# Kernel tuning notes

Measured on AMD Instinct MI355X. Metric: run time of the kernel, lower is better.

Reference implementation:

```python
import jax, jax.numpy as jnp
import numpy as np

D_MODEL = 1024
NUM_HEADS = 16
D_FF = 4096
EPS = 1e-5


def setup_inputs() -> dict:
    key = jax.random.key(0)
    ks = jax.random.split(key, 8)
    B, S, D = 4, 2048, D_MODEL
    s = 1.0 / np.sqrt(D)
    return {
        "x": jax.random.normal(ks[0], (B, S, D), jnp.float32),
        "ln1_w": jnp.ones((D,), jnp.float32),
        "ln2_w": jnp.ones((D,), jnp.float32),
        "wq": jax.random.normal(ks[1], (D, D), jnp.float32) * s,
        "wk": jax.random.normal(ks[2], (D, D), jnp.float32) * s,
        "wv": jax.random.normal(ks[3], (D, D), jnp.float32) * s,
        "wo": jax.random.normal(ks[4], (D, D), jnp.float32) * s,
        "w1": jax.random.normal(ks[5], (D_FF, D), jnp.float32) * s,
        "w2": jax.random.normal(ks[6], (D, D_FF), jnp.float32) * (1.0 / np.sqrt(D_FF)),
    }


def rmsnorm(a, w):
    # (a * w) / sqrt(mean(a^2) + eps)  -- matches torch module exactly
    denom = jnp.sqrt(jnp.mean(jnp.square(a), axis=-1, keepdims=True) + EPS)
    return a * w / denom


def attention(x, wq, wk, wv, wo):
    B, S, D = x.shape
    H, dk = NUM_HEADS, D // NUM_HEADS
    q = (x @ wq.T).reshape(B, S, H, dk).transpose(0, 2, 1, 3)  # B H S dk
    k = (x @ wk.T).reshape(B, S, H, dk).transpose(0, 2, 1, 3)
    v = (x @ wv.T).reshape(B, S, H, dk).transpose(0, 2, 1, 3)
    scores = jnp.einsum("bhqd,bhkd->bhqk", q, k) / np.sqrt(dk)
    causal = jnp.triu(jnp.ones((S, S), bool), k=1)
    scores = jnp.where(causal, -jnp.inf, scores)
    probs = jax.nn.softmax(scores, axis=-1)
    out = jnp.einsum("bhqk,bhkd->bhqd", probs, v)
    out = out.transpose(0, 2, 1, 3).reshape(B, S, D)
    return out @ wo.T


def ffn(x, w1, w2):
    h = x @ w1.T
    h = 0.5 * h * (1.0 + jax.lax.erf(h / np.sqrt(2.0).astype(np.float32)))
    return h @ w2.T


def reference(x, ln1_w, ln2_w, wq, wk, wv, wo, w1, w2):
    y = x + attention(rmsnorm(x, ln1_w), wq, wk, wv, wo)
    return y + ffn(rmsnorm(y, ln2_w), w1, w2)
```

## Files before the change

kernel.cpp:

```cpp
#include <hip/hip_runtime.h>

#define DM    1024
#define DFF   4096
#define SEQ   2048
#define BATCH 4
#define NROWS (BATCH * SEQ)
#define HEADS 16
#define DKH   64
#define KSTR  (2 * DM)

typedef __attribute__((ext_vector_type(4))) float          f32x4;
typedef __attribute__((ext_vector_type(8))) __bf16         bf16x8;
typedef __attribute__((ext_vector_type(8))) unsigned short u16x8;
typedef __attribute__((ext_vector_type(4))) unsigned short u16x4;

static __device__ __forceinline__ unsigned short f2bf(float f) {
  unsigned u = __builtin_bit_cast(unsigned, f);
  u += 0x7fffu + ((u >> 16) & 1u);
  return (unsigned short)(u >> 16);
}

__global__ void k_f2bf(const float* __restrict__ in, unsigned short* __restrict__ out, int n4) {
  int i = blockIdx.x * blockDim.x + threadIdx.x;
  if (i >= n4) return;
  float4 v = reinterpret_cast<const float4*>(in)[i];
  ushort4 o;
  o.x = f2bf(v.x); o.y = f2bf(v.y); o.z = f2bf(v.z); o.w = f2bf(v.w);
  reinterpret_cast<ushort4*>(out)[i] = o;
}

__global__ __launch_bounds__(256) void k_rmsnorm(const float* __restrict__ x,
                                                 const float* __restrict__ w,
                                                 unsigned short* __restrict__ out) {
  const int row = blockIdx.x;
  const float4 v = reinterpret_cast<const float4*>(x + (size_t)row * DM)[threadIdx.x];
  float ss = v.x * v.x + v.y * v.y + v.z * v.z + v.w * v.w;
#pragma unroll
  for (int off = 32; off > 0; off >>= 1) ss += __shfl_down(ss, off);
  __shared__ float red[4];
  if ((threadIdx.x & 63) == 0) red[threadIdx.x >> 6] = ss;
  __syncthreads();
  const float tot  = red[0] + red[1] + red[2] + red[3];
  const float rden = rsqrtf(tot * (1.0f / DM) + 1e-5f);
  const float4 wv = reinterpret_cast<const float4*>(w)[threadIdx.x];
  ushort4 o;
  o.x = f2bf(v.x * wv.x * rden);
  o.y = f2bf(v.y * wv.y * rden);
  o.z = f2bf(v.z * wv.z * rden);
  o.w = f2bf(v.w * wv.w * rden);
  reinterpret_cast<ushort4*>(out + (size_t)row * DM)[threadIdx.x] = o;
}

template <int EPI, int TN, int BK>
__global__ __launch_bounds__(256, 2) void k_gemm_nt(const unsigned short* __restrict__ A,
                                                    const unsigned short* __restrict__ B,
                                                    void* __restrict__ Cv,
                                                    const float* __restrict__ res,
                                                    int M, int N, int K) {
  constexpr int NW = TN / 128;
  alignas(16) __shared__ unsigned short As[2][128 * BK];
  alignas(16) __shared__ unsigned short Bs[2][128 * NW * BK];
  const int t  = threadIdx.x;
  const int w  = t >> 6;
  const int l  = t & 63;
  const int wr = w >> 1, wc = w & 1;
  const int lr = l & 15, lk = l >> 4;

  const unsigned bid = blockIdx.y * gridDim.x + blockIdx.x;
  const unsigned cpx = (gridDim.x * gridDim.y) >> 3;
  const unsigned sw  = (bid & 7) * cpx + (bid >> 3);
  const int m0 = (int)(sw / gridDim.x) * 128;
  const int n0 = (int)(sw % gridDim.x) * TN;

  auto stage = [&](int buf, int k0) {
    if constexpr (BK == 32) {
      const int srow = t >> 2;
      const int sgr  = (t & 3) ^ (srow & 3);
#pragma unroll
      for (int r = 0; r < 2; ++r) {
        const unsigned short* ga = A + (size_t)(m0 + r * 64 + srow) * K + k0 + 8 * sgr;
        __builtin_amdgcn_global_load_lds((__attribute__((address_space(1))) void*)ga,
                                         (__attribute__((address_space(3))) void*)(&As[buf][r * 2048 + w * 512]),
                                         16, 0, 0);
      }
#pragma unroll
      for (int r = 0; r < 2 * NW; ++r) {
        const unsigned short* gb = B + (size_t)(n0 + r * 64 + srow) * K + k0 + 8 * sgr;
        __builtin_amdgcn_global_load_lds((__attribute__((address_space(1))) void*)gb,
                                         (__attribute__((address_space(3))) void*)(&Bs[buf][r * 2048 + w * 512]),
                                         16, 0, 0);
      }
    } else {
      const int srow8 = l >> 3;
      const int g     = l & 7;
#pragma unroll
      for (int i = 0; i < 4; ++i) {
        const int row = i * 32 + w * 8 + srow8;
        const int sg  = g ^ (row & 7);
        const unsigned short* ga = A + (size_t)(m0 + row) * K + k0 + 8 * sg;
        __builtin_amdgcn_global_load_lds((__attribute__((address_space(1))) void*)ga,
                                         (__attribute__((address_space(3))) void*)(&As[buf][i * 2048 + w * 512]),
                                         16, 0, 0);
        const unsigned short* gb = B + (size_t)(n0 + row) * K + k0 + 8 * sg;
        __builtin_amdgcn_global_load_lds((__attribute__((address_space(1))) void*)gb,
                                         (__attribute__((address_space(3))) void*)(&Bs[buf][i * 2048 + w * 512]),
                                         16, 0, 0);
      }
    }
  };

  f32x4 acc[4][4 * NW] = {};

  stage(0, 0);
  const int nIt = K / BK;
  for (int it = 0; it < nIt; ++it) {
    const int buf = it & 1;
    __syncthreads();
    if (it + 1 < nIt) stage(buf ^ 1, (it + 1) * BK);

    if constexpr (BK == 32) {
      bf16x8 af[4], bf[4 * NW];
#pragma unroll
      for (int m = 0; m < 4; ++m)
        af[m] = *reinterpret_cast<const bf16x8*>(
            &As[buf][(wr * 64 + m * 16 + lr) * 32 + 8 * (lk ^ (lr & 3))]);
#pragma unroll
      for (int n = 0; n < 4 * NW; ++n)
        bf[n] = *reinterpret_cast<const bf16x8*>(
            &Bs[buf][(wc * 64 * NW + n * 16 + lr) * 32 + 8 * (lk ^ (lr & 3))]);
#pragma unroll
      for (int m = 0; m < 4; ++m)
#pragma unroll
        for (int n = 0; n < 4 * NW; ++n)
          acc[m][n] = __builtin_amdgcn_mfma_f32_16x16x32_bf16(af[m], bf[n], acc[m][n], 0, 0, 0);
    } else {
#pragma unroll
      for (int kk = 0; kk < 2; ++kk) {
        bf16x8 af[4], bf[4];
#pragma unroll
        for (int m = 0; m < 4; ++m)
          af[m] = *reinterpret_cast<const bf16x8*>(
              &As[buf][(wr * 64 + m * 16 + lr) * 64 + 8 * ((4 * kk + lk) ^ (lr & 7))]);
#pragma unroll
        for (int n = 0; n < 4; ++n)
          bf[n] = *reinterpret_cast<const bf16x8*>(
              &Bs[buf][(wc * 64 + n * 16 + lr) * 64 + 8 * ((4 * kk + lk) ^ (lr & 7))]);
#pragma unroll
        for (int m = 0; m < 4; ++m)
#pragma unroll
          for (int n = 0; n < 4; ++n)
            acc[m][n] = __builtin_amdgcn_mfma_f32_16x16x32_bf16(af[m], bf[n], acc[m][n], 0, 0, 0);
      }
    }
  }

#pragma unroll
  for (int m = 0; m < 4; ++m) {
#pragma unroll
    for (int n = 0; n < 4 * NW; ++n) {
#pragma unroll
      for (int r = 0; r < 4; ++r) {
        const size_t row = (size_t)(m0 + wr * 64 + m * 16 + lk * 4 + r);
        const size_t col = (size_t)(n0 + wc * 64 * NW + n * 16 + lr);
        const float a = acc[m][n][r];
        if constexpr (EPI == 0) {
          ((unsigned short*)Cv)[row * N + col] = f2bf(a);
        } else if constexpr (EPI == 1) {
          ((float*)Cv)[row * N + col] = a + res[row * N + col];
        } else if constexpr (EPI == 2) {
          const float h2 = a * a;
          const float e  = exp2f(a * (2.30221535f + 0.10295355f * h2));
          const float g  = a - a / (e + 1.0f);
          ((unsigned short*)Cv)[row * N + col] = f2bf(g);
        } else {
          const float sc = (col < DM) ? 0.18033688011f : 1.0f;
          ((unsigned short*)Cv)[row * N + col] = f2bf(a * sc);
        }
      }
    }
  }
}

__global__ __launch_bounds__(256, 3) void k_attn(const unsigned short* __restrict__ QK,
                                                 const unsigned short* __restrict__ VT,
                                                 unsigned short* __restrict__ O) {
  const int h   = blockIdx.x;
  const int qtA = blockIdx.y;
  const int qtB = 31 - qtA;
  const int b   = blockIdx.z;
  const int t  = threadIdx.x, w = t >> 6, l = t & 63;
  const int lr = l & 15, lk = l >> 4;
  const size_t rowB = (size_t)b * SEQ;
  const int hoff  = h * DKH;
  const int qw2[2] = { qtA * 64 + 16 * w, qtB * 64 + 16 * w };

  alignas(16) __shared__ unsigned short Ks[2][64 * 64];
  alignas(16) __shared__ unsigned short Vt[2][64 * 64];
  alignas(16) __shared__ unsigned short Ps[2][4][16 * 64];

  char* const KsB = (char*)Ks;
  char* const VtB = (char*)Vt;

  auto stage = [&](int buf, int kb2) {
#pragma unroll
    for (int half = 0; half < 2; ++half) {
      const int srow = w * 16 + half * 8 + (l >> 3);
      const int sgr  = (l & 7) ^ (srow & 7);
      const unsigned short* gk = QK + (size_t)(rowB + kb2 + srow) * KSTR + DM + hoff + 8 * sgr;
      __builtin_amdgcn_global_load_lds((__attribute__((address_space(1))) void*)gk,
                                       (__attribute__((address_space(3))) void*)(KsB + buf * 8192 + w * 2048 + half * 1024),
                                       16, 0, 0);
      const unsigned short* gv = VT + (size_t)(hoff + srow) * NROWS + rowB + kb2 + 8 * sgr;
      __builtin_amdgcn_global_load_lds((__attribute__((address_space(1))) void*)gv,
                                       (__attribute__((address_space(3))) void*)(VtB + buf * 8192 + w * 2048 + half * 1024),
                                       16, 0, 0);
    }
  };

  bf16x8 qf[2][2];
#pragma unroll
  for (int s = 0; s < 2; ++s)
#pragma unroll
    for (int kk = 0; kk < 2; ++kk)
      qf[s][kk] = *reinterpret_cast<const bf16x8*>(
          QK + (rowB + qw2[s] + lr) * KSTR + hoff + 32 * kk + 8 * lk);

  f32x4 oacc[2][4] = {};
  float mrun[2] = {-1e30f, -1e30f};
  float lrun[2] = {0.0f, 0.0f};

  const int ktmax = qtB;
  stage(0, 0);
  for (int kt = 0; kt <= ktmax; ++kt) {
    const int kbase = kt * 64;
    const int cur   = kt & 1;
    __syncthreads();
    if (kt < ktmax) stage(cur ^ 1, kbase + 64);
    const char* Kc = KsB + cur * 8192;
    const char* Vc = VtB + cur * 8192;

    const bool act[2] = { kbase <= qw2[0] + 15, kbase <= qw2[1] + 15 };

    f32x4 sacc[2][4] = {};
#pragma unroll
    for (int tt = 0; tt < 4; ++tt) {
      bf16x8 kf0 = *reinterpret_cast<const bf16x8*>(Kc + (16 * tt + lr) * 128 + 16 * ((lk + 0) ^ (lr & 7)));
      bf16x8 kf1 = *reinterpret_cast<const bf16x8*>(Kc + (16 * tt + lr) * 128 + 16 * ((lk + 4) ^ (lr & 7)));
#pragma unroll
      for (int s = 0; s < 2; ++s) {
        if (!act[s]) continue;
        sacc[s][tt] = __builtin_amdgcn_mfma_f32_16x16x32_bf16(kf0, qf[s][0], sacc[s][tt], 0, 0, 0);
        sacc[s][tt] = __builtin_amdgcn_mfma_f32_16x16x32_bf16(kf1, qf[s][1], sacc[s][tt], 0, 0, 0);
      }
    }

#pragma unroll
    for (int s = 0; s < 2; ++s) {
      if (!act[s]) continue;
      const int qw = qw2[s];
      char* const PsSB = (char*)(Ps[s][w]);
      const int qg = qw + lr;
      float sv[4][4];
      if (kbase + 63 > qw) {
#pragma unroll
        for (int tt = 0; tt < 4; ++tt)
#pragma unroll
          for (int r = 0; r < 4; ++r) {
            const int kg = kbase + 16 * tt + 4 * lk + r;
            sv[tt][r] = (kg > qg) ? -1e30f : sacc[s][tt][r];
          }
      } else {
#pragma unroll
        for (int tt = 0; tt < 4; ++tt)
#pragma unroll
          for (int r = 0; r < 4; ++r) sv[tt][r] = sacc[s][tt][r];
      }
      float tm = sv[0][0];
#pragma unroll
      for (int tt = 0; tt < 4; ++tt)
#pragma unroll
        for (int r = 0; r < 4; ++r) tm = fmaxf(tm, sv[tt][r]);
      tm = fmaxf(tm, __shfl_xor(tm, 16));
      tm = fmaxf(tm, __shfl_xor(tm, 32));
      float mref = mrun[s];
      if (__any(tm > mref + 8.0f)) {
        const float mnew  = fmaxf(mref, tm);
        const float alpha = exp2f(mref - mnew);
#pragma unroll
        for (int r = 0; r < 4; ++r) {
          const float ar = __shfl(alpha, 4 * lk + r);
#pragma unroll
          for (int dn = 0; dn < 4; ++dn) oacc[s][dn][r] *= ar;
        }
        lrun[s] *= alpha;
        mrun[s] = mnew;
        mref = mnew;
      }
      float ts = 0.0f;
      unsigned short pb[4][4];
#pragma unroll
      for (int tt = 0; tt < 4; ++tt)
#pragma unroll
        for (int r = 0; r < 4; ++r) {
          const float p = exp2f(sv[tt][r] - mref);
          ts += p;
          pb[tt][r] = __builtin_bit_cast(unsigned short, static_cast<__bf16>(p));
        }
      ts += __shfl_xor(ts, 16);
      ts += __shfl_xor(ts, 32);
      lrun[s] += ts;
#pragma unroll
      for (int tt = 0; tt < 4; ++tt) {
        u16x4 pw = {pb[tt][0], pb[tt][1], pb[tt][2], pb[tt][3]};
        *reinterpret_cast<u16x4*>(
            PsSB + lr * 128 + ((32 * tt + 8 * lk) ^ (16 * (lr & 7)))) = pw;
      }
    }

    asm volatile("" ::: "memory");

#pragma unroll
    for (int kk = 0; kk < 2; ++kk) {
      bf16x8 vf[4];
#pragma unroll
      for (int dn = 0; dn < 4; ++dn)
        vf[dn] = *reinterpret_cast<const bf16x8*>(
            Vc + (16 * dn + lr) * 128 + 16 * ((4 * kk + lk) ^ (lr & 7)));
#pragma unroll
      for (int s = 0; s < 2; ++s) {
        if (!act[s]) continue;
        char* const PsSB = (char*)(Ps[s][w]);
        bf16x8 pa = *reinterpret_cast<const bf16x8*>(
            PsSB + lr * 128 + ((64 * kk + 16 * lk) ^ (16 * (lr & 7))));
#pragma unroll
        for (int dn = 0; dn < 4; ++dn)
          oacc[s][dn] = __builtin_amdgcn_mfma_f32_16x16x32_bf16(pa, vf[dn], oacc[s][dn], 0, 0, 0);
      }
    }

    asm volatile("" ::: "memory");
  }

#pragma unroll
  for (int s = 0; s < 2; ++s)
#pragma unroll
    for (int r = 0; r < 4; ++r) {
      const float li = 1.0f / __shfl(lrun[s], 4 * lk + r);
      const size_t row = rowB + qw2[s] + 4 * lk + r;
#pragma unroll
      for (int dn = 0; dn < 4; ++dn)
        O[row * DM + hoff + 16 * dn + lr] = f2bf(oacc[s][dn][r] * li);
    }
}

extern "C" void kernel_launch(void* const* d_in, const int* in_sizes, int n_in,
                              void* d_out, int out_size, void* d_ws, size_t ws_size,
                              hipStream_t stream) {
  const float* x   = (const float*)d_in[0];
  const float* ln1 = (const float*)d_in[1];
  const float* ln2 = (const float*)d_in[2];
  const float* wq  = (const float*)d_in[3];
  const float* wk  = (const float*)d_in[4];
  const float* wv  = (const float*)d_in[5];
  const float* wo  = (const float*)d_in[6];
  const float* w1  = (const float*)d_in[7];
  const float* w2  = (const float*)d_in[8];

  char* ws = (char*)d_ws;
  size_t off = 0;
  auto take = [&](size_t bytes) { void* p = ws + off; off += bytes; return p; };
  unsigned short* wqkb = (unsigned short*)take((size_t)2 * DM * DM * 2);
  unsigned short* wvb  = (unsigned short*)take((size_t)DM * DM * 2);
  unsigned short* wob  = (unsigned short*)take((size_t)DM * DM * 2);
  unsigned short* w1b  = (unsigned short*)take((size_t)DFF * DM * 2);
  unsigned short* w2b  = (unsigned short*)take((size_t)DM * DFF * 2);
  unsigned short* qk   = (unsigned short*)take((size_t)NROWS * 2 * DM * 2);
  unsigned short* xn   = (unsigned short*)take((size_t)NROWS * DM * 2);
  unsigned short* vtb  = (unsigned short*)take((size_t)DM * NROWS * 2);
  float*          yb   = (float*)take((size_t)NROWS * DM * 4);
  unsigned short* hb   = (unsigned short*)take((size_t)NROWS * DFF * 2);
  unsigned short* yn   = qk;

  auto cvt = [&](const float* src, unsigned short* dst, size_t n) {
    int n4 = (int)(n / 4);
    k_f2bf<<<dim3((n4 + 255) / 256), dim3(256), 0, stream>>>(src, dst, n4);
  };
  cvt(wq, wqkb, (size_t)DM * DM);
  cvt(wk, wqkb + (size_t)DM * DM, (size_t)DM * DM);
  cvt(wv, wvb, (size_t)DM * DM);
  cvt(wo, wob, (size_t)DM * DM);
  cvt(w1, w1b, (size_t)DFF * DM);
  cvt(w2, w2b, (size_t)DM * DFF);

  k_rmsnorm<<<dim3(NROWS), dim3(256), 0, stream>>>(x, ln1, xn);

  k_gemm_nt<3, 256, 32><<<dim3(2 * DM / 256, NROWS / 128), dim3(256), 0, stream>>>(
      xn, wqkb, qk, nullptr, NROWS, 2 * DM, DM);

  k_gemm_nt<0, 128, 64><<<dim3(NROWS / 128, DM / 128), dim3(256), 0, stream>>>(
      wvb, xn, vtb, nullptr, DM, NROWS, DM);

  k_attn<<<dim3(HEADS, 16, BATCH), dim3(256), 0, stream>>>(qk, vtb, xn);

  k_gemm_nt<1, 128, 64><<<dim3(DM / 128, NROWS / 128), dim3(256), 0, stream>>>(
      xn, wob, yb, x, NROWS, DM, DM);

  k_rmsnorm<<<dim3(NROWS), dim3(256), 0, stream>>>(yb, ln2, yn);

  k_gemm_nt<2, 256, 32><<<dim3(DFF / 256, NROWS / 128), dim3(256), 0, stream>>>(
      yn, w1b, hb, nullptr, NROWS, DFF, DM);
  k_gemm_nt<1, 128, 64><<<dim3(DM / 128, NROWS / 128), dim3(256), 0, stream>>>(
      hb, w2b, (float*)d_out, yb, NROWS, DM, DFF);
}
```

Before: 391.0 us.

## Batch weight conversions into one launch, raise MFMA priority, tree-reduce softmax

Merges the six per-weight fp32-to-bf16 conversion launches into a single kernel that finds each thread's job from a cumulative-size table, removing per-launch overhead and tail effects. In the attention kernel, wraps the QK and PV MFMA sections in s_setprio raises so the scheduler favours matrix work across waves. It also rewrites the row-max and row-sum reductions as balanced trees to shorten dependency chains. The tree sum reorders float additions, which can change rounding slightly.

New measurement: 378.8 us. 1.03x faster.

```diff
diff --git a/kernel.cpp b/kernel.cpp
--- a/kernel.cpp
+++ b/kernel.cpp
@@ -20,13 +20,24 @@
   return (unsigned short)(u >> 16);
 }
 
-__global__ void k_f2bf(const float* __restrict__ in, unsigned short* __restrict__ out, int n4) {
-  int i = blockIdx.x * blockDim.x + threadIdx.x;
-  if (i >= n4) return;
-  float4 v = reinterpret_cast<const float4*>(in)[i];
+struct CvtJobs {
+  const float* src[6];
+  unsigned short* dst[6];
+};
+__constant__ const unsigned c_cum[6] = {262144u, 524288u, 786432u, 1048576u, 2097152u, 3145728u};
+
+__global__ __launch_bounds__(256) void k_f2bf_all(CvtJobs jobs) {
+  unsigned i = blockIdx.x * blockDim.x + threadIdx.x;
+  if (i >= 3145728u) return;
+  int j = 0;
+#pragma unroll
+  for (int s = 0; s < 6; ++s) j += (i >= c_cum[s]) ? 1 : 0;
+  const unsigned base = (j == 0) ? 0u : c_cum[j - 1];
+  const unsigned loc  = i - base;
+  float4 v = reinterpret_cast<const float4*>(jobs.src[j])[loc];
   ushort4 o;
   o.x = f2bf(v.x); o.y = f2bf(v.y); o.z = f2bf(v.z); o.w = f2bf(v.w);
-  reinterpret_cast<ushort4*>(out)[i] = o;
+  reinterpret_cast<ushort4*>(jobs.dst[j])[loc] = o;
 }
 
 __global__ __launch_bounds__(256) void k_rmsnorm(const float* __restrict__ x,
@@ -242,6 +253,7 @@
     const bool act[2] = { kbase <= qw2[0] + 15, kbase <= qw2[1] + 15 };
 
     f32x4 sacc[2][4] = {};
+    __builtin_amdgcn_s_setprio(1);
 #pragma unroll
     for (int tt = 0; tt < 4; ++tt) {
       bf16x8 kf0 = *reinterpret_cast<const bf16x8*>(Kc + (16 * tt + lr) * 128 + 16 * ((lk + 0) ^ (lr & 7)));
@@ -253,6 +265,7 @@
         sacc[s][tt] = __builtin_amdgcn_mfma_f32_16x16x32_bf16(kf1, qf[s][1], sacc[s][tt], 0, 0, 0);
       }
     }
+    __builtin_amdgcn_s_setprio(0);
 
 #pragma unroll
     for (int s = 0; s < 2; ++s) {
@@ -275,11 +288,12 @@
 #pragma unroll
           for (int r = 0; r < 4; ++r) sv[tt][r] = sacc[s][tt][r];
       }
-      float tm = sv[0][0];
-#pragma unroll
-      for (int tt = 0; tt < 4; ++tt)
-#pragma unroll
-        for (int r = 0; r < 4; ++r) tm = fmaxf(tm, sv[tt][r]);
+      const float a0 = fmaxf(fmaxf(sv[0][0], sv[0][1]), sv[0][2]);
+      const float a1 = fmaxf(fmaxf(sv[0][3], sv[1][0]), sv[1][1]);
+      const float a2 = fmaxf(fmaxf(sv[1][2], sv[1][3]), sv[2][0]);
+      const float a3 = fmaxf(fmaxf(sv[2][1], sv[2][2]), sv[2][3]);
+      const float a4 = fmaxf(fmaxf(sv[3][0], sv[3][1]), sv[3][2]);
+      float tm = fmaxf(fmaxf(fmaxf(a0, a1), a2), fmaxf(fmaxf(a3, a4), sv[3][3]));
       tm = fmaxf(tm, __shfl_xor(tm, 16));
       tm = fmaxf(tm, __shfl_xor(tm, 32));
       float mref = mrun[s];
@@ -296,16 +310,20 @@
         mrun[s] = mnew;
         mref = mnew;
       }
-      float ts = 0.0f;
+      float p[4][4];
       unsigned short pb[4][4];
 #pragma unroll
       for (int tt = 0; tt < 4; ++tt)
 #pragma unroll
         for (int r = 0; r < 4; ++r) {
-          const float p = exp2f(sv[tt][r] - mref);
-          ts += p;
-          pb[tt][r] = __builtin_bit_cast(unsigned short, static_cast<__bf16>(p));
+          p[tt][r] = exp2f(sv[tt][r] - mref);
+          pb[tt][r] = __builtin_bit_cast(unsigned short, static_cast<__bf16>(p[tt][r]));
         }
+      float t0 = (p[0][0] + p[0][1]) + (p[0][2] + p[0][3]);
+      float t1 = (p[1][0] + p[1][1]) + (p[1][2] + p[1][3]);
+      float t2 = (p[2][0] + p[2][1]) + (p[2][2] + p[2][3]);
+      float t3 = (p[3][0] + p[3][1]) + (p[3][2] + p[3][3]);
+      float ts = (t0 + t1) + (t2 + t3);
       ts += __shfl_xor(ts, 16);
       ts += __shfl_xor(ts, 32);
       lrun[s] += ts;
@@ -326,6 +344,7 @@
       for (int dn = 0; dn < 4; ++dn)
         vf[dn] = *reinterpret_cast<const bf16x8*>(
             Vc + (16 * dn + lr) * 128 + 16 * ((4 * kk + lk) ^ (lr & 7)));
+      __builtin_amdgcn_s_setprio(1);
 #pragma unroll
       for (int s = 0; s < 2; ++s) {
         if (!act[s]) continue;
@@ -336,6 +355,7 @@
         for (int dn = 0; dn < 4; ++dn)
           oacc[s][dn] = __builtin_amdgcn_mfma_f32_16x16x32_bf16(pa, vf[dn], oacc[s][dn], 0, 0, 0);
       }
+      __builtin_amdgcn_s_setprio(0);
     }
 
     asm volatile("" ::: "memory");
@@ -381,16 +401,14 @@
   unsigned short* hb   = (unsigned short*)take((size_t)NROWS * DFF * 2);
   unsigned short* yn   = qk;
 
-  auto cvt = [&](const float* src, unsigned short* dst, size_t n) {
-    int n4 = (int)(n / 4);
-    k_f2bf<<<dim3((n4 + 255) / 256), dim3(256), 0, stream>>>(src, dst, n4);
-  };
-  cvt(wq, wqkb, (size_t)DM * DM);
-  cvt(wk, wqkb + (size_t)DM * DM, (size_t)DM * DM);
-  cvt(wv, wvb, (size_t)DM * DM);
-  cvt(wo, wob, (size_t)DM * DM);
-  cvt(w1, w1b, (size_t)DFF * DM);
-  cvt(w2, w2b, (size_t)DM * DFF);
+  CvtJobs jobs;
+  jobs.src[0] = wq;  jobs.dst[0] = wqkb;
+  jobs.src[1] = wk;  jobs.dst[1] = wqkb + (size_t)DM * DM;
+  jobs.src[2] = wv;  jobs.dst[2] = wvb;
+  jobs.src[3] = wo;  jobs.dst[3] = wob;
+  jobs.src[4] = w1;  jobs.dst[4] = w1b;
+  jobs.src[5] = w2;  jobs.dst[5] = w2b;
+  k_f2bf_all<<<dim3(3145728u / 256u), dim3(256), 0, stream>>>(jobs);
 
   k_rmsnorm<<<dim3(NROWS), dim3(256), 0, stream>>>(x, ln1, xn);
 
```
